# Optimization experiments

Measured on AMD Instinct MI355X. Metric: run time of the kernel, lower is better.

Reference implementation:

```python
import jax, jax.numpy as jnp
import numpy as np

B, S, D, F, V, R = 4, 1024, 768, 3072, 2048, 8


def setup_inputs() -> dict:
    key = jax.random.key(0)
    k_x, k_r, k_w1, k_b1, k_w2, k_b2 = jax.random.split(key, 6)
    e_two = jax.random.normal(k_x, (B, S, D), dtype=jnp.float32)
    route_ids = jax.random.randint(k_r, (B, S), 0, R, dtype=jnp.int32)
    # Per-route classification head params (stacked over route axis R).
    W1 = jax.random.normal(k_w1, (R, D, F), dtype=jnp.float32) / np.sqrt(D)
    b1 = jnp.zeros((R, F), dtype=jnp.float32)
    W2 = jax.random.normal(k_w2, (R, F, V), dtype=jnp.float32) / np.sqrt(F)
    b2 = jnp.zeros((R, V), dtype=jnp.float32)
    return {"e_two": e_two, "route_ids": route_ids,
            "W1": W1, "b1": b1, "W2": W2, "b2": b2}


def reference(e_two, route_ids, W1, b1, W2, b2):
    # Each token goes through the MLP classification head selected by its
    # route_id:  softmax(relu(x @ W1[r] + b1[r]) @ W2[r] + b2[r]).
    # Dense formulation: run every route head over all tokens (R is a small
    # fixed set), then gather each token's own route output.
    h = jax.nn.relu(jnp.einsum('bsd,rdf->rbsf', e_two, W1)
                    + b1[:, None, None, :])            # [R,B,S,F]
    logits_all = jnp.einsum('rbsf,rfv->rbsv', h, W2) + b2[:, None, None, :]
    # Select per-token route: [R,B,S,V] -> [B,S,R,V] -> gather along R.
    logits_all = jnp.moveaxis(logits_all, 0, 2)        # [B,S,R,V]
    idx = route_ids[:, :, None, None].astype(jnp.int32)  # [B,S,1,1]
    logits = jnp.take_along_axis(logits_all, idx, axis=2)[:, :, 0, :]  # [B,S,V]
    return jax.nn.softmax(logits, axis=-1)
```

## Files before the change

kernel.cpp:

```cpp
#include <hip/hip_runtime.h>


typedef __attribute__((ext_vector_type(8))) short    s16x8;
typedef __attribute__((ext_vector_type(4))) float    f32x4;

#define T_TOK 4096
#define D_    768
#define F_    3072
#define V_    2048
#define R_    8
#define BM    128
#define BN    128
#define BK    64
#define MAXTILES 40
#define PADROWS  5120

#define OFF_COUNTS  ((size_t)0)
#define OFF_CURS    ((size_t)64)
#define OFF_PADOFF  ((size_t)128)
#define OFF_NT      ((size_t)192)
#define OFF_TROUTE  ((size_t)256)
#define OFF_TROW    ((size_t)512)
#define OFF_TOK     ((size_t)1024)
#define OFF_XG      ((size_t)32768)
#define OFF_H       (OFF_XG  + (size_t)PADROWS*D_*2)
#define OFF_W1T     (OFF_H   + (size_t)PADROWS*F_*2)
#define OFF_W2T     (OFF_W1T + (size_t)R_*F_*D_*2)

static __device__ __forceinline__ unsigned short f2bf(float f) {
  union { float f; unsigned int u; } x; x.f = f;
  unsigned int r = x.u + 0x7FFFu + ((x.u >> 16) & 1u);
  return (unsigned short)(r >> 16);
}

static __device__ __forceinline__ void gload_lds16(const unsigned short* g,
                                                   unsigned short* l) {
  __builtin_amdgcn_global_load_lds(
      (const __attribute__((address_space(1))) unsigned int*)(const void*)g,
      (__attribute__((address_space(3))) unsigned int*)(void*)l, 16, 0, 0);
}

__global__ void cr_count(const int* __restrict__ route, int* __restrict__ counts) {
  int t = blockIdx.x * blockDim.x + threadIdx.x;
  if (t < T_TOK) atomicAdd(&counts[route[t]], 1);
}

__global__ void cr_plan(const int* __restrict__ counts, int* __restrict__ padOff,
                        int* __restrict__ nTiles, int* __restrict__ tRoute,
                        int* __restrict__ tRow) {
  if (threadIdx.x != 0 || blockIdx.x != 0) return;
  int off = 0, tiles = 0;
  for (int r = 0; r < R_; ++r) {
    padOff[r] = off;
    int nt = (counts[r] + BM - 1) / BM;
    for (int i = 0; i < nt; ++i) { tRoute[tiles] = r; tRow[tiles] = off + i * BM; ++tiles; }
    off += nt * BM;
  }
  padOff[R_] = off;
  *nTiles = tiles;
}

__global__ void cr_scatter(const float* __restrict__ X, const int* __restrict__ route,
                           const int* __restrict__ padOff, int* __restrict__ curs,
                           int* __restrict__ tok, unsigned short* __restrict__ Xg) {
  __shared__ int spos;
  int t = blockIdx.x;
  if (threadIdx.x == 0) {
    int r = route[t];
    int p = padOff[r] + atomicAdd(&curs[r], 1);
    tok[p] = t;
    spos = p;
  }
  __syncthreads();
  int pos = spos;
  float4 v = reinterpret_cast<const float4*>(X + (size_t)t * D_)[threadIdx.x];
  ushort4 o;
  o.x = f2bf(v.x); o.y = f2bf(v.y); o.z = f2bf(v.z); o.w = f2bf(v.w);
  *reinterpret_cast<ushort4*>(Xg + (size_t)pos * D_ + threadIdx.x * 4) = o;
}

template <int K, int N>
__global__ void cr_transpose(const float* __restrict__ W, unsigned short* __restrict__ Wt) {
  __shared__ float tile[64][65];
  int r = blockIdx.z;
  const float* Wr = W + (size_t)r * K * N;
  unsigned short* Wtr = Wt + (size_t)r * N * K;
  int k0 = blockIdx.x * 64, n0 = blockIdx.y * 64;
  int t = threadIdx.x;
  int cb = (t & 15) * 4, rb = t >> 4;
#pragma unroll
  for (int i = 0; i < 4; ++i) {
    int k = rb + i * 16;
    float4 v = *reinterpret_cast<const float4*>(Wr + (size_t)(k0 + k) * N + n0 + cb);
    tile[k][cb] = v.x; tile[k][cb + 1] = v.y; tile[k][cb + 2] = v.z; tile[k][cb + 3] = v.w;
  }
  __syncthreads();
  int n = t >> 2, kc = (t & 3) * 16;
  alignas(16) unsigned short o[16];
#pragma unroll
  for (int j = 0; j < 16; ++j) o[j] = f2bf(tile[kc + j][n]);
  unsigned short* dst = Wtr + (size_t)(n0 + n) * K + k0 + kc;
  *reinterpret_cast<s16x8*>(dst)     = *reinterpret_cast<const s16x8*>(&o[0]);
  *reinterpret_cast<s16x8*>(dst + 8) = *reinterpret_cast<const s16x8*>(&o[8]);
}

template <int K, int N, int MODE>
__global__ __launch_bounds__(256) void cr_gemm(
    const unsigned short* __restrict__ A, const unsigned short* __restrict__ Wt,
    const float* __restrict__ bias, const int* __restrict__ nTiles,
    const int* __restrict__ tRoute, const int* __restrict__ tRow,
    const int* __restrict__ tok, unsigned short* __restrict__ Hout,
    float* __restrict__ Fout) {
  int mt = blockIdx.x;
  if (mt >= *nTiles) return;
  int route = tRoute[mt], row0 = tRow[mt];
  int col0 = blockIdx.y * BN;
  const unsigned short* Ag = A + (size_t)row0 * K;
  const unsigned short* Bg = Wt + ((size_t)route * N + col0) * K;

  __shared__ __align__(16) unsigned short As[BM * BK];
  __shared__ __align__(16) unsigned short Bs[BN * BK];

  int tid = threadIdx.x, lane = tid & 63, w = tid >> 6;
  int wr = w >> 1, wc = w & 1;
  int srow = lane >> 3;
  int scol = (lane & 7) * 8;
  int frow = lane & 15;
  int fk   = (lane >> 4) * 8;

  f32x4 acc[4][4] = {};

  for (int kt = 0; kt < K; kt += BK) {
#pragma unroll
    for (int j = 0; j < 4; ++j) {
      int chunk = j * 4 + w;
      int rrow = chunk * 8 + srow;
      gload_lds16(Ag + (size_t)rrow * K + kt + scol, As + chunk * 512);
      gload_lds16(Bg + (size_t)rrow * K + kt + scol, Bs + chunk * 512);
    }
    __syncthreads();
#pragma unroll
    for (int kk = 0; kk < 2; ++kk) {
      s16x8 a[4], b[4];
#pragma unroll
      for (int mi = 0; mi < 4; ++mi)
        a[mi] = *reinterpret_cast<const s16x8*>(&As[(wr * 64 + mi * 16 + frow) * BK + kk * 32 + fk]);
#pragma unroll
      for (int ni = 0; ni < 4; ++ni)
        b[ni] = *reinterpret_cast<const s16x8*>(&Bs[(wc * 64 + ni * 16 + frow) * BK + kk * 32 + fk]);
#pragma unroll
      for (int mi = 0; mi < 4; ++mi)
#pragma unroll
        for (int ni = 0; ni < 4; ++ni)
          acc[mi][ni] = __builtin_amdgcn_mfma_f32_16x16x32_bf16(a[mi], b[ni], acc[mi][ni], 0, 0, 0);
    }
    __syncthreads();
  }

  int crow = (lane >> 4) * 4;
  int ccol = lane & 15;
#pragma unroll
  for (int mi = 0; mi < 4; ++mi) {
#pragma unroll
    for (int ni = 0; ni < 4; ++ni) {
      int gcol = col0 + wc * 64 + ni * 16 + ccol;
      float bv = bias[(size_t)route * N + gcol];
#pragma unroll
      for (int j = 0; j < 4; ++j) {
        int prow = row0 + wr * 64 + mi * 16 + crow + j;
        float v = acc[mi][ni][j] + bv;
        if (MODE == 0) {
          v = fmaxf(v, 0.f);
          Hout[(size_t)prow * N + gcol] = f2bf(v);
        } else {
          int tk = tok[prow];
          if (tk >= 0) Fout[(size_t)tk * N + gcol] = v;
        }
      }
    }
  }
}

__global__ void cr_softmax(float* __restrict__ out) {
  int row = blockIdx.x;
  float* p = out + (size_t)row * V_;
  int t = threadIdx.x;
  float4 v0 = reinterpret_cast<float4*>(p)[t];
  float4 v1 = reinterpret_cast<float4*>(p)[t + 256];
  float m = fmaxf(fmaxf(fmaxf(v0.x, v0.y), fmaxf(v0.z, v0.w)),
                  fmaxf(fmaxf(v1.x, v1.y), fmaxf(v1.z, v1.w)));
#pragma unroll
  for (int o = 32; o; o >>= 1) m = fmaxf(m, __shfl_xor(m, o));
  __shared__ float sm[4], ss[4];
  int w = t >> 6;
  if ((t & 63) == 0) sm[w] = m;
  __syncthreads();
  m = fmaxf(fmaxf(sm[0], sm[1]), fmaxf(sm[2], sm[3]));
  v0.x = expf(v0.x - m); v0.y = expf(v0.y - m); v0.z = expf(v0.z - m); v0.w = expf(v0.w - m);
  v1.x = expf(v1.x - m); v1.y = expf(v1.y - m); v1.z = expf(v1.z - m); v1.w = expf(v1.w - m);
  float s = v0.x + v0.y + v0.z + v0.w + v1.x + v1.y + v1.z + v1.w;
#pragma unroll
  for (int o = 32; o; o >>= 1) s += __shfl_xor(s, o);
  if ((t & 63) == 0) ss[w] = s;
  __syncthreads();
  s = ss[0] + ss[1] + ss[2] + ss[3];
  float inv = 1.f / s;
  v0.x *= inv; v0.y *= inv; v0.z *= inv; v0.w *= inv;
  v1.x *= inv; v1.y *= inv; v1.z *= inv; v1.w *= inv;
  reinterpret_cast<float4*>(p)[t] = v0;
  reinterpret_cast<float4*>(p)[t + 256] = v1;
}

extern "C" void kernel_launch(void* const* d_in, const int* in_sizes, int n_in,
                              void* d_out, int out_size, void* d_ws, size_t ws_size,
                              hipStream_t stream) {
  const float* X      = (const float*)d_in[0];
  const int*   route  = (const int*)d_in[1];
  const float* W1     = (const float*)d_in[2];
  const float* b1     = (const float*)d_in[3];
  const float* W2     = (const float*)d_in[4];
  const float* b2     = (const float*)d_in[5];
  float*       out    = (float*)d_out;
  char*        ws     = (char*)d_ws;

  int* counts = (int*)(ws + OFF_COUNTS);
  int* curs   = (int*)(ws + OFF_CURS);
  int* padOff = (int*)(ws + OFF_PADOFF);
  int* nT     = (int*)(ws + OFF_NT);
  int* tRoute = (int*)(ws + OFF_TROUTE);
  int* tRow   = (int*)(ws + OFF_TROW);
  int* tok    = (int*)(ws + OFF_TOK);
  unsigned short* Xg  = (unsigned short*)(ws + OFF_XG);
  unsigned short* H   = (unsigned short*)(ws + OFF_H);
  unsigned short* W1T = (unsigned short*)(ws + OFF_W1T);
  unsigned short* W2T = (unsigned short*)(ws + OFF_W2T);

  hipMemsetAsync(ws, 0, 1024, stream);
  hipMemsetAsync(ws + OFF_TOK, 0xFF, (size_t)PADROWS * 4, stream);
  hipMemsetAsync(ws + OFF_XG, 0, (size_t)PADROWS * D_ * 2, stream);

  cr_count<<<T_TOK / 256, 256, 0, stream>>>(route, counts);
  cr_plan<<<1, 64, 0, stream>>>(counts, padOff, nT, tRoute, tRow);
  cr_scatter<<<T_TOK, 192, 0, stream>>>(X, route, padOff, curs, tok, Xg);

  cr_transpose<D_, F_><<<dim3(D_ / 64, F_ / 64, R_), 256, 0, stream>>>(W1, W1T);
  cr_transpose<F_, V_><<<dim3(F_ / 64, V_ / 64, R_), 256, 0, stream>>>(W2, W2T);

  cr_gemm<D_, F_, 0><<<dim3(MAXTILES, F_ / BN), 256, 0, stream>>>(
      Xg, W1T, b1, nT, tRoute, tRow, tok, H, nullptr);
  cr_gemm<F_, V_, 1><<<dim3(MAXTILES, V_ / BN), 256, 0, stream>>>(
      H, W2T, b2, nT, tRoute, tRow, tok, nullptr, out);

  cr_softmax<<<T_TOK, 256, 0, stream>>>(out);
}
```

Baseline: 650.8 us.

## Add split-K to second GEMM, XOR-swizzle LDS tiles, widen transpose tiles

The second GEMM now splits K into two slices and accumulates into the zeroed output with float atomics. Its bias moves into the softmax kernel. Both GEMMs use a 1D grid, and LDS tile loads use an XOR swizzle to cut bank conflicts on the fragment reads. The weight transpose now handles 128-row tiles per block. The split-K adds parallelism to the second GEMM (40×16 tiles) at the cost of an extra output memset and atomic traffic, and the workspace offsets move to make room for larger tile tables.

```diff
diff --git a/kernel.cpp b/kernel.cpp
--- a/kernel.cpp
+++ b/kernel.cpp
@@ -20,8 +20,8 @@
 #define OFF_PADOFF  ((size_t)128)
 #define OFF_NT      ((size_t)192)
 #define OFF_TROUTE  ((size_t)256)
-#define OFF_TROW    ((size_t)512)
-#define OFF_TOK     ((size_t)1024)
+#define OFF_TROW    ((size_t)1024)
+#define OFF_TOK     ((size_t)4096)
 #define OFF_XG      ((size_t)32768)
 #define OFF_H       (OFF_XG  + (size_t)PADROWS*D_*2)
 #define OFF_W1T     (OFF_H   + (size_t)PADROWS*F_*2)
@@ -81,62 +81,77 @@
 
 template <int K, int N>
 __global__ void cr_transpose(const float* __restrict__ W, unsigned short* __restrict__ Wt) {
-  __shared__ float tile[64][65];
+  __shared__ float tile[128][65];
   int r = blockIdx.z;
   const float* Wr = W + (size_t)r * K * N;
   unsigned short* Wtr = Wt + (size_t)r * N * K;
-  int k0 = blockIdx.x * 64, n0 = blockIdx.y * 64;
+  int k0 = blockIdx.x * 128, n0 = blockIdx.y * 64;
   int t = threadIdx.x;
   int cb = (t & 15) * 4, rb = t >> 4;
 #pragma unroll
-  for (int i = 0; i < 4; ++i) {
+  for (int i = 0; i < 8; ++i) {
     int k = rb + i * 16;
     float4 v = *reinterpret_cast<const float4*>(Wr + (size_t)(k0 + k) * N + n0 + cb);
     tile[k][cb] = v.x; tile[k][cb + 1] = v.y; tile[k][cb + 2] = v.z; tile[k][cb + 3] = v.w;
   }
   __syncthreads();
-  int n = t >> 2, kc = (t & 3) * 16;
-  alignas(16) unsigned short o[16];
-#pragma unroll
-  for (int j = 0; j < 16; ++j) o[j] = f2bf(tile[kc + j][n]);
-  unsigned short* dst = Wtr + (size_t)(n0 + n) * K + k0 + kc;
-  *reinterpret_cast<s16x8*>(dst)     = *reinterpret_cast<const s16x8*>(&o[0]);
-  *reinterpret_cast<s16x8*>(dst + 8) = *reinterpret_cast<const s16x8*>(&o[8]);
-}
-
-template <int K, int N, int MODE>
+  int nl = t >> 3, kc = (t & 7) * 16;
+#pragma unroll
+  for (int np = 0; np < 2; ++np) {
+    int n = nl + np * 32;
+    alignas(16) unsigned short o[16];
+#pragma unroll
+    for (int j = 0; j < 16; ++j) o[j] = f2bf(tile[kc + j][n]);
+    unsigned short* dst = Wtr + (size_t)(n0 + n) * K + k0 + kc;
+    *reinterpret_cast<s16x8*>(dst)     = *reinterpret_cast<const s16x8*>(&o[0]);
+    *reinterpret_cast<s16x8*>(dst + 8) = *reinterpret_cast<const s16x8*>(&o[8]);
+  }
+}
+
+template <int K, int N, int MODE, int KSLICES>
 __global__ __launch_bounds__(256) void cr_gemm(
     const unsigned short* __restrict__ A, const unsigned short* __restrict__ Wt,
     const float* __restrict__ bias, const int* __restrict__ nTiles,
     const int* __restrict__ tRoute, const int* __restrict__ tRow,
     const int* __restrict__ tok, unsigned short* __restrict__ Hout,
     float* __restrict__ Fout) {
-  int mt = blockIdx.x;
+  constexpr int NY = N / BN;
+  constexpr int KS_LEN = K / KSLICES;
+  int bid = blockIdx.x;
+  int ks  = bid / (MAXTILES * NY);
+  int rem = bid - ks * (MAXTILES * NY);
+  int y   = rem / MAXTILES;
+  int mt  = rem - y * MAXTILES;
   if (mt >= *nTiles) return;
   int route = tRoute[mt], row0 = tRow[mt];
-  int col0 = blockIdx.y * BN;
-  const unsigned short* Ag = A + (size_t)row0 * K;
-  const unsigned short* Bg = Wt + ((size_t)route * N + col0) * K;
+  int col0 = y * BN;
+  int kbase = ks * KS_LEN;
+  const unsigned short* Ag = A + (size_t)row0 * K + kbase;
+  const unsigned short* Bg = Wt + ((size_t)route * N + col0) * K + kbase;
 
   __shared__ __align__(16) unsigned short As[BM * BK];
   __shared__ __align__(16) unsigned short Bs[BN * BK];
 
   int tid = threadIdx.x, lane = tid & 63, w = tid >> 6;
   int wr = w >> 1, wc = w & 1;
-  int srow = lane >> 3;
-  int scol = (lane & 7) * 8;
+  int rl = lane >> 3;
+  int kx = ((lane & 7) ^ rl) * 8;
   int frow = lane & 15;
   int fk   = (lane >> 4) * 8;
+  int rx   = (frow & 7) << 3;
 
   f32x4 acc[4][4] = {};
 
-  for (int kt = 0; kt < K; kt += BK) {
+  for (int kt = 0; kt < KS_LEN; kt += BK) {
 #pragma unroll
     for (int j = 0; j < 4; ++j) {
-      int chunk = j * 4 + w;
-      int rrow = chunk * 8 + srow;
-      gload_lds16(Ag + (size_t)rrow * K + kt + scol, As + chunk * 512);
-      gload_lds16(Bg + (size_t)rrow * K + kt + scol, Bs + chunk * 512);
+      int c = j * 4 + w;
+      gload_lds16(Ag + (size_t)(c * 8 + rl) * K + kt + kx, As + c * 512);
+    }
+#pragma unroll
+    for (int j = 0; j < 4; ++j) {
+      int c = j * 4 + w;
+      gload_lds16(Bg + (size_t)(c * 8 + rl) * K + kt + kx, Bs + c * 512);
     }
     __syncthreads();
 #pragma unroll
@@ -144,15 +159,18 @@
       s16x8 a[4], b[4];
 #pragma unroll
       for (int mi = 0; mi < 4; ++mi)
-        a[mi] = *reinterpret_cast<const s16x8*>(&As[(wr * 64 + mi * 16 + frow) * BK + kk * 32 + fk]);
+        a[mi] = *reinterpret_cast<const s16x8*>(
+            &As[(wr * 64 + mi * 16 + frow) * BK + ((kk * 32 + fk) ^ rx)]);
 #pragma unroll
       for (int ni = 0; ni < 4; ++ni)
-        b[ni] = *reinterpret_cast<const s16x8*>(&Bs[(wc * 64 + ni * 16 + frow) * BK + kk * 32 + fk]);
+        b[ni] = *reinterpret_cast<const s16x8*>(
+            &Bs[(wc * 64 + ni * 16 + frow) * BK + ((kk * 32 + fk) ^ rx)]);
 #pragma unroll
       for (int mi = 0; mi < 4; ++mi)
 #pragma unroll
         for (int ni = 0; ni < 4; ++ni)
-          acc[mi][ni] = __builtin_amdgcn_mfma_f32_16x16x32_bf16(a[mi], b[ni], acc[mi][ni], 0, 0, 0);
+          acc[mi][ni] = __builtin_amdgcn_mfma_f32_16x16x32_bf16(
+              a[mi], b[ni], acc[mi][ni], 0, 0, 0);
     }
     __syncthreads();
   }
@@ -164,29 +182,35 @@
 #pragma unroll
     for (int ni = 0; ni < 4; ++ni) {
       int gcol = col0 + wc * 64 + ni * 16 + ccol;
-      float bv = bias[(size_t)route * N + gcol];
 #pragma unroll
       for (int j = 0; j < 4; ++j) {
         int prow = row0 + wr * 64 + mi * 16 + crow + j;
-        float v = acc[mi][ni][j] + bv;
+        float v = acc[mi][ni][j];
         if (MODE == 0) {
-          v = fmaxf(v, 0.f);
+          v = fmaxf(v + bias[(size_t)route * N + gcol], 0.f);
           Hout[(size_t)prow * N + gcol] = f2bf(v);
         } else {
           int tk = tok[prow];
-          if (tk >= 0) Fout[(size_t)tk * N + gcol] = v;
+          if (tk >= 0) atomicAdd(&Fout[(size_t)tk * N + gcol], v);
         }
       }
     }
   }
 }
 
-__global__ void cr_softmax(float* __restrict__ out) {
+__global__ void cr_softmax(float* __restrict__ out, const int* __restrict__ route,
+                           const float* __restrict__ b2) {
   int row = blockIdx.x;
+  int r = route[row];
   float* p = out + (size_t)row * V_;
+  const float* bp = b2 + (size_t)r * V_;
   int t = threadIdx.x;
   float4 v0 = reinterpret_cast<float4*>(p)[t];
   float4 v1 = reinterpret_cast<float4*>(p)[t + 256];
+  float4 b0 = reinterpret_cast<const float4*>(bp)[t];
+  float4 b1 = reinterpret_cast<const float4*>(bp)[t + 256];
+  v0.x += b0.x; v0.y += b0.y; v0.z += b0.z; v0.w += b0.w;
+  v1.x += b1.x; v1.y += b1.y; v1.z += b1.z; v1.w += b1.w;
   float m = fmaxf(fmaxf(fmaxf(v0.x, v0.y), fmaxf(v0.z, v0.w)),
                   fmaxf(fmaxf(v1.x, v1.y), fmaxf(v1.z, v1.w)));
 #pragma unroll
@@ -235,21 +259,22 @@
   unsigned short* W1T = (unsigned short*)(ws + OFF_W1T);
   unsigned short* W2T = (unsigned short*)(ws + OFF_W2T);
 
-  hipMemsetAsync(ws, 0, 1024, stream);
+  hipMemsetAsync(ws, 0, 4096, stream);
   hipMemsetAsync(ws + OFF_TOK, 0xFF, (size_t)PADROWS * 4, stream);
   hipMemsetAsync(ws + OFF_XG, 0, (size_t)PADROWS * D_ * 2, stream);
+  hipMemsetAsync(out, 0, (size_t)T_TOK * V_ * 4, stream);
 
   cr_count<<<T_TOK / 256, 256, 0, stream>>>(route, counts);
   cr_plan<<<1, 64, 0, stream>>>(counts, padOff, nT, tRoute, tRow);
   cr_scatter<<<T_TOK, 192, 0, stream>>>(X, route, padOff, curs, tok, Xg);
 
-  cr_transpose<D_, F_><<<dim3(D_ / 64, F_ / 64, R_), 256, 0, stream>>>(W1, W1T);
-  cr_transpose<F_, V_><<<dim3(F_ / 64, V_ / 64, R_), 256, 0, stream>>>(W2, W2T);
-
-  cr_gemm<D_, F_, 0><<<dim3(MAXTILES, F_ / BN), 256, 0, stream>>>(
+  cr_transpose<D_, F_><<<dim3(D_ / 128, F_ / 64, R_), 256, 0, stream>>>(W1, W1T);
+  cr_transpose<F_, V_><<<dim3(F_ / 128, V_ / 64, R_), 256, 0, stream>>>(W2, W2T);
+
+  cr_gemm<D_, F_, 0, 1><<<MAXTILES * (F_ / BN), 256, 0, stream>>>(
       Xg, W1T, b1, nT, tRoute, tRow, tok, H, nullptr);
-  cr_gemm<F_, V_, 1><<<dim3(MAXTILES, V_ / BN), 256, 0, stream>>>(
-      H, W2T, b2, nT, tRoute, tRow, tok, nullptr, out);
-
-  cr_softmax<<<T_TOK, 256, 0, stream>>>(out);
-}
+  cr_gemm<F_, V_, 1, 2><<<MAXTILES * (V_ / BN) * 2, 256, 0, stream>>>(
+      H, W2T, nullptr, nT, tRoute, tRow, tok, nullptr, out);
+
+  cr_softmax<<<T_TOK, 256, 0, stream>>>(out, route, b2);
+}
```

After: 639.9 us. No clear change (-1.7%).
